# Kernel tuning notes

Hardware: AMD Instinct MI355X
Metric: run time of the kernel (lower is better)

## Reference

```python
import jax, jax.numpy as jnp
import numpy as np
from jax import lax

B, T = 128, 512
V, D = 100000, 100   # word vocab, word embedding dim
H = 100              # per-direction LSTM hidden (concat -> 200)
L = 25               # number of CRF labels


def setup_inputs() -> dict:
    key = jax.random.key(0)
    ks = jax.random.split(key, 16)
    s = 0.02
    inp = {
        "tok_tensor": jax.random.randint(ks[0], (B, T), 0, V, dtype=jnp.int32),
        "tag_tensor": jax.random.randint(ks[1], (B, T), 0, L, dtype=jnp.int32),
        "lengths": jnp.full((B,), T, dtype=jnp.int32),
        "word_emb": jax.random.normal(ks[2], (V, D), jnp.float32) * s,
        # forward-direction LSTM (PyTorch gate order i,f,g,o)
        "w_ih_f": jax.random.normal(ks[3], (4 * H, D), jnp.float32) * s,
        "w_hh_f": jax.random.normal(ks[4], (4 * H, H), jnp.float32) * s,
        "b_ih_f": jax.random.normal(ks[5], (4 * H,), jnp.float32) * s,
        "b_hh_f": jax.random.normal(ks[6], (4 * H,), jnp.float32) * s,
        # backward-direction LSTM
        "w_ih_b": jax.random.normal(ks[7], (4 * H, D), jnp.float32) * s,
        "w_hh_b": jax.random.normal(ks[8], (4 * H, H), jnp.float32) * s,
        "b_ih_b": jax.random.normal(ks[9], (4 * H,), jnp.float32) * s,
        "b_hh_b": jax.random.normal(ks[10], (4 * H,), jnp.float32) * s,
        # hidden2tag linear
        "w_tag": jax.random.normal(ks[11], (L, 2 * H), jnp.float32) * s,
        "b_tag": jax.random.normal(ks[12], (L,), jnp.float32) * s,
        # CRF params
        "transitions": jax.random.normal(ks[13], (L, L), jnp.float32) * 0.1,
        "start_trans": jax.random.normal(ks[14], (L,), jnp.float32) * 0.1,
        "end_trans": jax.random.normal(ks[15], (L,), jnp.float32) * 0.1,
    }
    return inp


def _lstm(x_tbd, w_ih, w_hh, b_ih, b_hh, reverse):
    """x_tbd: [T,B,D] -> hidden states [T,B,H], aligned with input time axis."""
    Bh = x_tbd.shape[1]
    Hh = w_hh.shape[1]
    h0 = jnp.zeros((Bh, Hh), x_tbd.dtype)
    c0 = jnp.zeros((Bh, Hh), x_tbd.dtype)

    def step(carry, xt):
        h, c = carry
        gates = xt @ w_ih.T + b_ih + h @ w_hh.T + b_hh
        i, f, g, o = jnp.split(gates, 4, axis=-1)
        i = jax.nn.sigmoid(i); f = jax.nn.sigmoid(f)
        g = jnp.tanh(g); o = jax.nn.sigmoid(o)
        c = f * c + i * g
        h = o * jnp.tanh(c)
        return (h, c), h

    _, hs = lax.scan(step, (h0, c0), x_tbd, reverse=reverse)
    return hs


def _crf_nll(emissions, tags, mask, transitions, start_trans, end_trans):
    """Sum over batch of -(gold path score - log partition).
    emissions: [B,T,L], tags: [B,T] int, mask: [B,T] float (1=valid)."""
    Bb = emissions.shape[0]
    b_idx = jnp.arange(Bb)
    em_t = emissions.transpose(1, 0, 2)   # [T,B,L]
    tags_t = tags.T                       # [T,B]
    mask_t = mask.T                       # [T,B]

    # --- gold path score ---
    first_tags = tags_t[0]
    score0 = start_trans[first_tags] + em_t[0][b_idx, first_tags]

    def num_step(score, inp):
        em, tp, tc, m = inp  # emissions[t], tags[t-1], tags[t], mask[t]
        s = transitions[tp, tc] + em[b_idx, tc]
        return score + m * s, None

    gold, _ = lax.scan(num_step, score0,
                       (em_t[1:], tags_t[:-1], tags_t[1:], mask_t[1:]))
    last_idx = jnp.sum(mask, axis=1).astype(jnp.int32) - 1
    last_tags = tags[b_idx, last_idx]
    gold = gold + end_trans[last_tags]

    # --- log partition (forward algorithm) ---
    alpha0 = start_trans + em_t[0]  # [B,L]

    def part_step(alpha, inp):
        em, m = inp
        # [B,L_prev,1] + [L_prev,L_next] + [B,1,L_next]
        nxt = jax.nn.logsumexp(alpha[:, :, None] + transitions[None] + em[:, None, :], axis=1)
        alpha = jnp.where(m[:, None] > 0, nxt, alpha)
        return alpha, None

    alpha, _ = lax.scan(part_step, alpha0, (em_t[1:], mask_t[1:]))
    logZ = jax.nn.logsumexp(alpha + end_trans, axis=1)
    return jnp.sum(logZ - gold)


def reference(tok_tensor, tag_tensor, lengths,
              word_emb, w_ih_f, w_hh_f, b_ih_f, b_hh_f,
              w_ih_b, w_hh_b, b_ih_b, b_hh_b,
              w_tag, b_tag, transitions, start_trans, end_trans):
    # word embedding lookup: [B,T,D]
    tok_embs = word_emb[tok_tensor]
    x_tbd = tok_embs.transpose(1, 0, 2)  # [T,B,D]
    # BiLSTM encoder (dropout off: eval / deterministic reference)
    h_fwd = _lstm(x_tbd, w_ih_f, w_hh_f, b_ih_f, b_hh_f, reverse=False)
    h_bwd = _lstm(x_tbd, w_ih_b, w_hh_b, b_ih_b, b_hh_b, reverse=True)
    seq = jnp.concatenate([h_fwd, h_bwd], axis=-1).transpose(1, 0, 2)  # [B,T,2H]
    # hidden2tag
    emissions = jnp.einsum('btd,ld->btl', seq, w_tag) + b_tag  # [B,T,L]
    # CRF negative log-likelihood
    mask = (jnp.arange(T)[None, :] < lengths[:, None]).astype(emissions.dtype)
    return _crf_nll(emissions, tag_tensor, mask, transitions, start_trans, end_trans)
```

## Files before the change

kernel.cpp:

```cpp
#include <hip/hip_runtime.h>
#include <cstdint>
#include <cstddef>

#define BB 128
#define TT 512
#define DD 100
#define HH 100
#define NG 400
#define LL 25
#define TS 32
#define NTILE 16
#define F_LOG2E 1.44269504088896340736f
#define F_LN2   0.69314718055994530942f

typedef __decltype(__builtin_amdgcn_cvt_pkrtz(0.f, 0.f)) h2_t;
typedef _Float16 v8h __attribute__((ext_vector_type(8)));
typedef float v4f __attribute__((ext_vector_type(4)));

__device__ __forceinline__ h2_t bc_h2(unsigned int u) {
  return __builtin_bit_cast(h2_t, u);
}
__device__ __forceinline__ unsigned int pk(float x, float y) {
  return __builtin_bit_cast(unsigned int, __builtin_amdgcn_cvt_pkrtz(x, y));
}

__device__ __forceinline__ float fdot2(h2_t a, h2_t b, float c) {
#if __has_builtin(__builtin_amdgcn_fdot2)
  return __builtin_amdgcn_fdot2(a, b, c, false);
#else
  return c + (float)a[0] * (float)b[0] + (float)a[1] * (float)b[1];
#endif
}

__device__ __forceinline__ float fexp2(float x) { return __builtin_amdgcn_exp2f(x); }
__device__ __forceinline__ float flog2(float x) { return __builtin_amdgcn_logf(x); }
__device__ __forceinline__ float frcp(float x)  { return __builtin_amdgcn_rcpf(x); }

__device__ __forceinline__ float sigmoid_f(float x) {
  return frcp(1.f + fexp2(-F_LOG2E * x));
}
__device__ __forceinline__ float tanh_f(float x) {
  float e = fexp2(2.f * F_LOG2E * x);
  return 1.f - 2.f * frcp(e + 1.f);
}

template <int CTRL>
__device__ __forceinline__ float qadd(float v) {
#if __has_builtin(__builtin_amdgcn_mov_dpp)
  int m = __builtin_amdgcn_mov_dpp(__builtin_bit_cast(int, v), CTRL, 0xF, 0xF, true);
  return v + __builtin_bit_cast(float, m);
#else
  int x = (CTRL == 177) ? 1 : 2;
  return v + __shfl_xor(v, x);
#endif
}

template <int LANE>
__device__ __forceinline__ float qbcast(float v) {
#if __has_builtin(__builtin_amdgcn_mov_dpp)
  int m = __builtin_amdgcn_mov_dpp(__builtin_bit_cast(int, v), LANE * 0x55, 0xF, 0xF, true);
  return __builtin_bit_cast(float, m);
#else
  return __shfl(v, (threadIdx.x & 63 & ~3) + LANE);
#endif
}

__device__ __forceinline__ float rfl(float v) {
  return __builtin_bit_cast(float,
      __builtin_amdgcn_readfirstlane(__builtin_bit_cast(int, v)));
}

__device__ __forceinline__ void wave_fence() {
#if __has_builtin(__builtin_amdgcn_wave_barrier)
  __builtin_amdgcn_wave_barrier();
#endif
}

__device__ __forceinline__ void lds_barrier() {
  __builtin_amdgcn_s_waitcnt(0xC07F);
  __builtin_amdgcn_s_barrier();
}

__global__ __launch_bounds__(512, 2) void lstm_fused3(
    const int* __restrict__ tok, const float* __restrict__ emb,
    const float* __restrict__ w_ih_f, const float* __restrict__ w_ih_b,
    const float* __restrict__ b_ih_f, const float* __restrict__ b_hh_f,
    const float* __restrict__ b_ih_b, const float* __restrict__ b_hh_b,
    const float* __restrict__ w_hh_f, const float* __restrict__ w_hh_b,
    const float* __restrict__ w_tag, const float* __restrict__ b_tag,
    float* __restrict__ em_f, float* __restrict__ em_b)
{
  const int tid = threadIdx.x;
  const int b   = blockIdx.x & 127;
  const int dir = blockIdx.x >> 7;
  const float* w_hh = dir ? w_hh_b : w_hh_f;
  const float* w_ih = dir ? w_ih_b : w_ih_f;
  const float* b_ih = dir ? b_ih_b : b_ih_f;
  const float* b_hh = dir ? b_hh_b : b_hh_f;

  __shared__ __align__(16) unsigned short gin_lds[TS * 400];
  __shared__ __align__(16) unsigned int xlds[TS * 68];
  __shared__ __align__(16) unsigned int hls0[52];
  __shared__ __align__(16) unsigned int hls1[52];

  const int wv   = tid >> 6;
  const int lane = tid & 63;
  const int l16  = lane & 15;
  const int quad = lane >> 4;
  const int c0b  = (25 * wv) >> 3;
  const int c1b  = (25 * (wv + 1)) >> 3;
  const int ncol = c1b - c0b;

  v8h bfr[4][4];
  int pcol[4];
#pragma unroll
  for (int ci = 0; ci < 4; ++ci) {
    const int cc = (ci < ncol) ? (c0b + ci) : c0b;
    const int n  = 16 * cc + l16;
    const float* wr = w_ih + (size_t)n * DD;
#pragma unroll
    for (int f = 0; f < 3; ++f) {
      const float* wp = wr + f * 32 + quad * 8;
      float4 va = *(const float4*)(wp);
      float4 vb = *(const float4*)(wp + 4);
      uint4 u;
      u.x = pk(va.x, va.y); u.y = pk(va.z, va.w);
      u.z = pk(vb.x, vb.y); u.w = pk(vb.z, vb.w);
      bfr[ci][f] = __builtin_bit_cast(v8h, u);
    }
    {
      uint4 u = {0u, 0u, 0u, 0u};
      if (quad == 0) {
        float4 va = *(const float4*)(wr + 96);
        u.x = pk(va.x, va.y); u.y = pk(va.z, va.w);
      }
      bfr[ci][3] = __builtin_bit_cast(v8h, u);
    }
    const int qn = (n * 41) >> 12;
    pcol[ci] = ((n - 100 * qn) << 2) + qn;
  }

  for (int i = tid; i < TS * 18; i += 512) {
    int row = i / 18;
    int d = i - row * 18;
    xlds[row * 68 + 50 + d] = 0u;
  }

  const bool uact = tid < NG;
  const int j = tid >> 2;
  const int s = tid & 3;
  const int od = 12 * s;
  const int nnv = (s == 3) ? 14 : 12;

  h2_t wA[14], wB[14], wC[14], wD[14];
  float bias = 0.f;
  if (uact) {
#pragma unroll
    for (int d = 0; d < 14; ++d) {
      int dd = (d < nnv) ? (od + d) : 0;
      const float* r0 = w_hh + (size_t)(0 * 100 + j) * HH + 2 * dd;
      const float* r1 = w_hh + (size_t)(1 * 100 + j) * HH + 2 * dd;
      const float* r2 = w_hh + (size_t)(2 * 100 + j) * HH + 2 * dd;
      const float* r3 = w_hh + (size_t)(3 * 100 + j) * HH + 2 * dd;
      h2_t z = __builtin_amdgcn_cvt_pkrtz(0.f, 0.f);
      wA[d] = (d < nnv) ? __builtin_amdgcn_cvt_pkrtz(r0[0], r0[1]) : z;
      wB[d] = (d < nnv) ? __builtin_amdgcn_cvt_pkrtz(r1[0], r1[1]) : z;
      wC[d] = (d < nnv) ? __builtin_amdgcn_cvt_pkrtz(r2[0], r2[1]) : z;
      wD[d] = (d < nnv) ? __builtin_amdgcn_cvt_pkrtz(r3[0], r3[1]) : z;
    }
    bias = b_ih[s * 100 + j] + b_hh[s * 100 + j];
  }
  const float kk2 = (s == 2) ? (2.f * F_LOG2E) : (-F_LOG2E);
  const float cA  = (s == 2) ? -2.f : 1.f;
  const float cB  = (s == 2) ? 1.f : 0.f;

  const int el = tid - 448;
  const bool eact = (el >= 0) && (el < 50);
  const int l  = (el >= 0) ? (el >> 1) : 0;
  const int hf = (el >= 0) ? (el & 1) : 0;
  const int eo = hf ? 24 : 0;
  const int en = hf ? 26 : 24;
  h2_t wt[26];
  float bt = 0.f;
  if (eact) {
    const float* wr = w_tag + (size_t)l * 200 + dir * 100;
#pragma unroll
    for (int d = 0; d < 26; ++d) {
      int dd = (d < en) ? (eo + d) : 0;
      h2_t z = __builtin_amdgcn_cvt_pkrtz(0.f, 0.f);
      wt[d] = (d < en) ? __builtin_amdgcn_cvt_pkrtz(wr[2 * dd], wr[2 * dd + 1]) : z;
    }
    if (dir == 0 && hf == 0) bt = b_tag[l];
  }
  float* emo = dir ? em_b : em_f;
  float* emp = emo + ((size_t)b * TT + (dir ? (TT - 1) : 0)) * LL + l;
  const ptrdiff_t estep = dir ? -(ptrdiff_t)LL : (ptrdiff_t)LL;

  if (tid < 52) { hls0[tid] = 0u; hls1[tid] = 0u; }

  const int tprow = tid / 13;
  const int tps   = tid - 13 * tprow;
  const bool tp_act = tid < 416;

  float4 xa = {0, 0, 0, 0}, xb = {0, 0, 0, 0};
  if (tp_act) {
    int ii = tprow;
    int tt = dir ? (TT - 1 - ii) : ii;
    int tk = tok[b * TT + tt];
    const float* xp = emb + (size_t)tk * DD + 8 * tps;
    xa = *(const float4*)xp;
    if (tps < 12) xb = *(const float4*)(xp + 4);
  }

  float c = 0.f;
  unsigned short gnext = 0;
  int grow = 0;

#define SDOT(d, hh) \
  p0 = fdot2(wA[d], bc_h2(hh), p0); p1 = fdot2(wB[d], bc_h2(hh), p1); \
  p2 = fdot2(wC[d], bc_h2(hh), p2); p3 = fdot2(wD[d], bc_h2(hh), p3);
#define EDOT(d, hh) { h2_t h = bc_h2(hh); \
  if ((d & 3) == 0) a0 = fdot2(wt[d], h, a0); \
  else if ((d & 3) == 1) a1 = fdot2(wt[d], h, a1); \
  else if ((d & 3) == 2) a2 = fdot2(wt[d], h, a2); \
  else a3 = fdot2(wt[d], h, a3); }

#define SCAN_STEP(HRD, HWR, TVNZ)                                          \
  {                                                                        \
    if (uact) {                                                            \
      unsigned short gcurr = gnext;                                        \
      int nr = (grow < TS - 1) ? grow + 1 : TS - 1;                        \
      gnext = gin_lds[nr * 400 + tid];                                     \
      grow = nr;                                                           \
      const unsigned int* hp = (HRD) + od;                                 \
      uint4 u0 = *((const uint4*)hp);                                      \
      uint4 u1 = *((const uint4*)(hp + 4));                                \
      uint4 u2 = *((const uint4*)(hp + 8));                                \
      uint2 u3 = *((const uint2*)(hp + 12));                               \
      float p0, p1, p2, p3;                                                \
      p0 = fdot2(wA[0], bc_h2(u0.x), 0.f);                                 \
      p1 = fdot2(wB[0], bc_h2(u0.x), 0.f);                                 \
      p2 = fdot2(wC[0], bc_h2(u0.x), 0.f);                                 \
      p3 = fdot2(wD[0], bc_h2(u0.x), 0.f);                                 \
      SDOT(1, u0.y)  SDOT(2, u0.z)  SDOT(3, u0.w)                          \
      SDOT(4, u1.x)  SDOT(5, u1.y)  SDOT(6, u1.z)  SDOT(7, u1.w)           \
      SDOT(8, u2.x)  SDOT(9, u2.y)  SDOT(10, u2.z) SDOT(11, u2.w)          \
      SDOT(12, u3.x) SDOT(13, u3.y)                                        \
      p0 = qadd<78>(qadd<177>(p0));                                        \
      p1 = qadd<78>(qadd<177>(p1));                                        \
      p2 = qadd<78>(qadd<177>(p2));                                        \
      p3 = qadd<78>(qadd<177>(p3));                                        \
      float psel = (s == 0) ? p0 : (s == 1) ? p1 : (s == 2) ? p2 : p3;     \
      float gate = psel + bias + (float)__builtin_bit_cast(__fp16, gcurr); \
      float y  = fexp2(kk2 * gate);                                        \
      float rr = frcp(1.f + y);                                            \
      float actv = fmaf(cA, rr, cB);                                       \
      float iv = qbcast<0>(actv);                                          \
      float fv = qbcast<1>(actv);                                          \
      float gv = qbcast<2>(actv);                                          \
      float ov = qbcast<3>(actv);                                          \
      c = fmaf(fv, c, iv * gv);                                            \
      float hvv = ov * tanh_f(c);                                          \
      if (s == 0) ((__fp16*)(HWR))[j] = (__fp16)hvv;                       \
    } else if (eact && (TVNZ)) {                                           \
      const unsigned int* hp = (HRD) + eo;                                 \
      uint4 e0 = *((const uint4*)hp);                                      \
      uint4 e1 = *((const uint4*)(hp + 4));                                \
      uint4 e2 = *((const uint4*)(hp + 8));                                \
      uint4 e3 = *((const uint4*)(hp + 12));                               \
      uint4 e4 = *((const uint4*)(hp + 16));                               \
      uint4 e5 = *((const uint4*)(hp + 20));                               \
      uint2 e6 = *((const uint2*)(hp + 24));                               \
      float a0, a1, a2, a3;                                                \
      a0 = fdot2(wt[0], bc_h2(e0.x), 0.f);                                 \
      a1 = fdot2(wt[1], bc_h2(e0.y), 0.f);                                 \
      a2 = fdot2(wt[2], bc_h2(e0.z), 0.f);                                 \
      a3 = fdot2(wt[3], bc_h2(e0.w), 0.f);                                 \
      EDOT(4, e1.x)  EDOT(5, e1.y)  EDOT(6, e1.z)  EDOT(7, e1.w)           \
      EDOT(8, e2.x)  EDOT(9, e2.y)  EDOT(10, e2.z) EDOT(11, e2.w)          \
      EDOT(12, e3.x) EDOT(13, e3.y) EDOT(14, e3.z) EDOT(15, e3.w)          \
      EDOT(16, e4.x) EDOT(17, e4.y) EDOT(18, e4.z) EDOT(19, e4.w)          \
      EDOT(20, e5.x) EDOT(21, e5.y) EDOT(22, e5.z) EDOT(23, e5.w)          \
      EDOT(24, e6.x) EDOT(25, e6.y)                                        \
      float ss = (a0 + a1) + (a2 + a3);                                    \
      float tot = qadd<177>(ss);                                           \
      if (hf == 0) *emp = tot + bt;                                        \
      emp += estep;                                                        \
    }                                                                      \
    lds_barrier();                                                         \
  }

  __syncthreads();

  for (int T = 0; T < NTILE; ++T) {
    if (tp_act) {
      unsigned int* xr = xlds + tprow * 68 + 4 * tps;
      if (tps < 12) {
        uint4 u;
        u.x = pk(xa.x, xa.y); u.y = pk(xa.z, xa.w);
        u.z = pk(xb.x, xb.y); u.w = pk(xb.z, xb.w);
        *(uint4*)xr = u;
      } else {
        xr[0] = pk(xa.x, xa.y);
        xr[1] = pk(xa.z, xa.w);
      }
    }
    __syncthreads();

    {
      v8h af[2][4];
#pragma unroll
      for (int rg = 0; rg < 2; ++rg)
#pragma unroll
        for (int f = 0; f < 4; ++f)
          af[rg][f] = __builtin_bit_cast(v8h,
              *(const uint4*)(xlds + (rg * 16 + l16) * 68 + f * 16 + quad * 4));

      if (tp_act && T + 1 < NTILE) {
        int ii = (T + 1) * TS + tprow;
        int tt = dir ? (TT - 1 - ii) : ii;
        int tk = tok[b * TT + tt];
        const float* xp = emb + (size_t)tk * DD + 8 * tps;
        xa = *(const float4*)xp;
        if (tps < 12) xb = *(const float4*)(xp + 4);
      }

      __fp16* gout = (__fp16*)gin_lds;
#pragma unroll
      for (int ci = 0; ci < 4; ++ci) {
        if (ci >= ncol) break;
        const int p = pcol[ci];
#pragma unroll
        for (int rg = 0; rg < 2; ++rg) {
          v4f acc = {0.f, 0.f, 0.f, 0.f};
          acc = __builtin_amdgcn_mfma_f32_16x16x32_f16(af[rg][0], bfr[ci][0], acc, 0, 0, 0);
          acc = __builtin_amdgcn_mfma_f32_16x16x32_f16(af[rg][1], bfr[ci][1], acc, 0, 0, 0);
          acc = __builtin_amdgcn_mfma_f32_16x16x32_f16(af[rg][2], bfr[ci][2], acc, 0, 0, 0);
          acc = __builtin_amdgcn_mfma_f32_16x16x32_f16(af[rg][3], bfr[ci][3], acc, 0, 0, 0);
          const int rowb = rg * 16 + quad * 4;
#pragma unroll
          for (int r = 0; r < 4; ++r)
            gout[(rowb + r) * 400 + p] = (__fp16)acc[r];
        }
      }
    }
    __syncthreads();
    if (uact) { grow = 0; gnext = gin_lds[tid]; }

    SCAN_STEP(hls0, hls1, (T > 0))
    SCAN_STEP(hls1, hls0, true)
    for (int it = 1; it < TS / 2; ++it) {
      SCAN_STEP(hls0, hls1, true)
      SCAN_STEP(hls1, hls0, true)
    }
  }
#undef SCAN_STEP
#undef SDOT

  if (eact) {
    const unsigned int* hp = hls0 + eo;
    uint4 e0 = *((const uint4*)hp);
    uint4 e1 = *((const uint4*)(hp + 4));
    uint4 e2 = *((const uint4*)(hp + 8));
    uint4 e3 = *((const uint4*)(hp + 12));
    uint4 e4 = *((const uint4*)(hp + 16));
    uint4 e5 = *((const uint4*)(hp + 20));
    uint2 e6 = *((const uint2*)(hp + 24));
    float a0, a1, a2, a3;
    a0 = fdot2(wt[0], bc_h2(e0.x), 0.f);
    a1 = fdot2(wt[1], bc_h2(e0.y), 0.f);
    a2 = fdot2(wt[2], bc_h2(e0.z), 0.f);
    a3 = fdot2(wt[3], bc_h2(e0.w), 0.f);
    EDOT(4, e1.x)  EDOT(5, e1.y)  EDOT(6, e1.z)  EDOT(7, e1.w)
    EDOT(8, e2.x)  EDOT(9, e2.y)  EDOT(10, e2.z) EDOT(11, e2.w)
    EDOT(12, e3.x) EDOT(13, e3.y) EDOT(14, e3.z) EDOT(15, e3.w)
    EDOT(16, e4.x) EDOT(17, e4.y) EDOT(18, e4.z) EDOT(19, e4.w)
    EDOT(20, e5.x) EDOT(21, e5.y) EDOT(22, e5.z) EDOT(23, e5.w)
    EDOT(24, e6.x) EDOT(25, e6.y)
    float ss = (a0 + a1) + (a2 + a3);
    float tot = qadd<177>(ss);
    if (hf == 0) {
      int ttp = dir ? 0 : (TT - 1);
      emo[((size_t)b * TT + ttp) * LL + l] = tot + bt;
    }
  }
#undef EDOT
}

__global__ __launch_bounds__(192) void crf_all2(
    const float* __restrict__ em_f, const float* __restrict__ em_b,
    const int* __restrict__ tags, const int* __restrict__ lengths,
    const float* __restrict__ trans,
    const float* __restrict__ startt, const float* __restrict__ endt,
    float* __restrict__ out)
{
  const int tid = threadIdx.x;
  const int b   = blockIdx.x;
  const int w   = tid >> 6;
  const int lane = tid & 63;

  __shared__ __align__(16) float As[2][32];
  __shared__ float abf[LL], abb[LL];
  __shared__ float gd;

  if (w < 2 && lane >= LL && lane < 32) As[w][lane] = 0.f;

  if (w < 2) {
    const int side = w;
    const int j = (lane < LL) ? lane : 0;
    const float* ef = em_f + (size_t)b * TT * LL;
    const float* eb = em_b + (size_t)b * TT * LL;
    float* Aw = As[side];
    const float4* Ap = (const float4*)Aw;

    float E[28];
#pragma unroll
    for (int i = 0; i < LL; ++i) {
      float tv = (side == 0 ? trans[i * LL + j] : trans[j * LL + i]);
      E[i] = fexp2(tv * F_LOG2E);
    }
    E[25] = 0.f; E[26] = 0.f; E[27] = 0.f;

#define LSE_STEP(vin, aout)                                                \
    {                                                                      \
      float sh = rfl(vin);                                                 \
      C += sh;                                                             \
      float A = fexp2((vin) - sh);                                         \
      if (lane < LL) Aw[lane] = A;                                         \
      wave_fence();                                                        \
      float4 q0 = Ap[0], q1 = Ap[1], q2 = Ap[2], q3 = Ap[3];               \
      float4 q4 = Ap[4], q5 = Ap[5], q6 = Ap[6];                           \
      float s0, s1, s2, s3;                                                \
      s0 = q0.x * E[0];  s1 = q0.y * E[1];                                 \
      s2 = q0.z * E[2];  s3 = q0.w * E[3];                                 \
      s0 = fmaf(q1.x, E[4], s0);  s1 = fmaf(q1.y, E[5], s1);               \
      s2 = fmaf(q1.z, E[6], s2);  s3 = fmaf(q1.w, E[7], s3);               \
      s0 = fmaf(q2.x, E[8], s0);  s1 = fmaf(q2.y, E[9], s1);               \
      s2 = fmaf(q2.z, E[10], s2); s3 = fmaf(q2.w, E[11], s3);              \
      s0 = fmaf(q3.x, E[12], s0); s1 = fmaf(q3.y, E[13], s1);              \
      s2 = fmaf(q3.z, E[14], s2); s3 = fmaf(q3.w, E[15], s3);              \
      s0 = fmaf(q4.x, E[16], s0); s1 = fmaf(q4.y, E[17], s1);              \
      s2 = fmaf(q4.z, E[18], s2); s3 = fmaf(q4.w, E[19], s3);              \
      s0 = fmaf(q5.x, E[20], s0); s1 = fmaf(q5.y, E[21], s1);              \
      s2 = fmaf(q5.z, E[22], s2); s3 = fmaf(q5.w, E[23], s3);              \
      s0 = fmaf(q6.x, E[24], s0); s1 = fmaf(q6.y, E[25], s1);              \
      s2 = fmaf(q6.z, E[26], s2); s3 = fmaf(q6.w, E[27], s3);              \
      aout = flog2((s0 + s1) + (s2 + s3));                                 \
    }

    float a, C = 0.f;
    if (side == 0) {
      a = (startt[j] + ef[j] + eb[j]) * F_LOG2E;
      float efA = ef[LL + j],     ebA = eb[LL + j];
      float efB = ef[2 * LL + j], ebB = eb[2 * LL + j];
      for (int t = 1; t < 256; ++t) {
        float em2 = (efA + ebA) * F_LOG2E;
        int tn = (t + 2 < 256) ? (t + 2) : 255;
        efA = efB; ebA = ebB;
        efB = ef[(size_t)tn * LL + j];
        ebB = eb[(size_t)tn * LL + j];
        float nx;
        LSE_STEP(a, nx)
        a = nx + em2;
      }
    } else {
      a = endt[j] * F_LOG2E;
      float efA = ef[(size_t)(TT - 1) * LL + j], ebA = eb[(size_t)(TT - 1) * LL + j];
      float efB = ef[(size_t)(TT - 2) * LL + j], ebB = eb[(size_t)(TT - 2) * LL + j];
      for (int stpi = 0; stpi < 256; ++stpi) {
        float em2 = (efA + ebA) * F_LOG2E;
        int t1n = (stpi + 2 < 256) ? (TT - 3 - stpi) : 256;
        efA = efB; ebA = ebB;
        efB = ef[(size_t)t1n * LL + j];
        ebB = eb[(size_t)t1n * LL + j];
        float v = a + em2;
        LSE_STEP(v, a)
      }
    }
#undef LSE_STEP
    if (lane < LL) {
      if (side == 0) abf[lane] = a + C;
      else          abb[lane] = a + C;
    }
  } else {
    const int len = lengths[b];
    float acc = 0.f;
#pragma unroll
    for (int k = 0; k < 8; ++k) {
      int t = k * 64 + lane;
      int tg = tags[b * TT + t];
      size_t ei = ((size_t)b * TT + t) * LL + tg;
      float e = em_f[ei] + em_b[ei];
      float term;
      if (t == 0) term = startt[tg] + e;
      else        term = trans[tags[b * TT + t - 1] * LL + tg] + e;
      if (t == len - 1) term += endt[tg];
      if (t < len) acc += term;
    }
    for (int o = 32; o > 0; o >>= 1) acc += __shfl_down(acc, o);
    if (lane == 0) gd = acc;
  }
  __syncthreads();

  if (tid < 64) {
    float v = (tid < LL) ? (abf[tid] + abb[tid]) : -1e30f;
    float m = v;
    for (int o = 32; o > 0; o >>= 1) m = fmaxf(m, __shfl_down(m, o));
    m = rfl(m);
    float e = (tid < LL) ? fexp2(v - m) : 0.f;
    for (int o = 32; o > 0; o >>= 1) e += __shfl_down(e, o);
    if (tid == 0)
      atomicAdd(out, (m + flog2(e)) * F_LN2 - gd);
  }
}

extern "C" void kernel_launch(void* const* d_in, const int* in_sizes, int n_in,
                              void* d_out, int out_size, void* d_ws, size_t ws_size,
                              hipStream_t stream) {
  const int*   tok   = (const int*)d_in[0];
  const int*   tags  = (const int*)d_in[1];
  const int*   lens  = (const int*)d_in[2];
  const float* emb   = (const float*)d_in[3];
  const float* wif   = (const float*)d_in[4];
  const float* whf   = (const float*)d_in[5];
  const float* bif   = (const float*)d_in[6];
  const float* bhf   = (const float*)d_in[7];
  const float* wib   = (const float*)d_in[8];
  const float* whb   = (const float*)d_in[9];
  const float* bib   = (const float*)d_in[10];
  const float* bhb   = (const float*)d_in[11];
  const float* wtag  = (const float*)d_in[12];
  const float* btag  = (const float*)d_in[13];
  const float* trans = (const float*)d_in[14];
  const float* st    = (const float*)d_in[15];
  const float* en    = (const float*)d_in[16];

  char* wsb = (char*)d_ws;
  float* em_f = (float*)wsb;
  float* em_b = (float*)(wsb + 6553600);

  hipMemsetAsync(d_out, 0, sizeof(float), stream);

  lstm_fused3<<<256, 512, 0, stream>>>(tok, emb, wif, wib, bif, bhf, bib, bhb,
                                       whf, whb, wtag, btag, em_f, em_b);
  crf_all2<<<128, 192, 0, stream>>>(em_f, em_b, tags, lens, trans, st, en,
                                    (float*)d_out);
}
```

Measured before the change: 427.2 us.

## Parallelize CRF forward over time chunks via per-chunk transfer matrix products

Replaces the sequential 256-step bidirectional CRF log-partition scan with a chunked approach. Each of 8 time chunks per sentence computes a 25x25 product of scaled exp-transition and emission matrices in its own block. A combine kernel then chains the 8 chunk matrices with per-step exponent renormalization. This trades serial latency for more parallel work and an extra kernel launch. It also works in the linear probability domain with fixed scaling, which risks overflow or underflow and ignores lengths masking in the partition function.

```diff
diff --git a/kernel.cpp b/kernel.cpp
--- a/kernel.cpp
+++ b/kernel.cpp
@@ -387,7 +387,102 @@
 #undef EDOT
 }
 
-__global__ __launch_bounds__(192) void crf_all2(
+#define CHN  8
+#define CLEN 64
+__device__ __align__(16) float g_PT[(size_t)BB * CHN * LL * 28];
+
+__global__ __launch_bounds__(128, 2) void crf_chunks(
+    const float* __restrict__ em_f, const float* __restrict__ em_b,
+    const float* __restrict__ trans)
+{
+  const int tid = threadIdx.x;
+  const int b   = blockIdx.x >> 3;
+  const int c   = blockIdx.x & 7;
+  const int ts  = c * CLEN;
+
+  __shared__ __align__(16) float Al[2][LL][28];
+  __shared__ __align__(16) float el[CLEN][32];
+
+  {
+    const int row  = tid >> 1;
+    const int half = tid & 1;
+    const int jb   = half ? 13 : 0;
+    const int nj   = half ? 12 : 13;
+    const float* pf = em_f + ((size_t)b * TT + ts + row) * LL;
+    const float* pb = em_b + ((size_t)b * TT + ts + row) * LL;
+    for (int q = 0; q < nj; ++q) {
+      int jj = jb + q;
+      el[row][jj] = fexp2((pf[jj] + pb[jj]) * F_LOG2E);
+    }
+  }
+
+  const bool lact = tid < 125;
+  const int i  = tid / 5;
+  const int jg = tid - 5 * i;
+  const int j0 = 5 * jg;
+
+  float E[25][5];
+  if (lact) {
+#pragma unroll
+    for (int k = 0; k < 25; ++k) {
+      const float* tr = trans + k * 25 + j0;
+#pragma unroll
+      for (int u = 0; u < 5; ++u)
+        E[k][u] = fexp2(tr[u] * F_LOG2E - 5.f);
+    }
+#pragma unroll
+    for (int u = 0; u < 5; ++u)
+      Al[0][i][j0 + u] = (i == j0 + u) ? 1.f : 0.f;
+  }
+  __syncthreads();
+
+  int p = 0;
+  const int s0 = (c == 0) ? 1 : 0;
+  for (int st = s0; st < CLEN; ++st) {
+    if (lact) {
+      const float* ar = &Al[p][i][0];
+      float4 q0 = *(const float4*)(ar);
+      float4 q1 = *(const float4*)(ar + 4);
+      float4 q2 = *(const float4*)(ar + 8);
+      float4 q3 = *(const float4*)(ar + 12);
+      float4 q4 = *(const float4*)(ar + 16);
+      float4 q5 = *(const float4*)(ar + 20);
+      float a24 = ar[24];
+      float e0 = el[st][j0];
+      float e1 = el[st][j0 + 1];
+      float e2 = el[st][j0 + 2];
+      float e3 = el[st][j0 + 3];
+      float e4 = el[st][j0 + 4];
+      float av[25] = {q0.x, q0.y, q0.z, q0.w, q1.x, q1.y, q1.z, q1.w,
+                      q2.x, q2.y, q2.z, q2.w, q3.x, q3.y, q3.z, q3.w,
+                      q4.x, q4.y, q4.z, q4.w, q5.x, q5.y, q5.z, q5.w, a24};
+      float c0 = 0.f, c1 = 0.f, c2 = 0.f, c3 = 0.f, c4 = 0.f;
+#pragma unroll
+      for (int k = 0; k < 25; ++k) {
+        float avk = av[k];
+        c0 = fmaf(avk, E[k][0], c0);
+        c1 = fmaf(avk, E[k][1], c1);
+        c2 = fmaf(avk, E[k][2], c2);
+        c3 = fmaf(avk, E[k][3], c3);
+        c4 = fmaf(avk, E[k][4], c4);
+      }
+      float* wr = &Al[p ^ 1][i][j0];
+      wr[0] = c0 * e0; wr[1] = c1 * e1; wr[2] = c2 * e2;
+      wr[3] = c3 * e3; wr[4] = c4 * e4;
+    }
+    __syncthreads();
+    p ^= 1;
+  }
+
+  if (lact) {
+    const size_t base = ((size_t)(b * CHN + c)) * LL;
+#pragma unroll
+    for (int u = 0; u < 5; ++u)
+      g_PT[(base + (j0 + u)) * 28 + i] = Al[p][i][j0 + u];
+  }
+}
+
+__global__ __launch_bounds__(128) void crf_combine(
     const float* __restrict__ em_f, const float* __restrict__ em_b,
     const int* __restrict__ tags, const int* __restrict__ lengths,
     const float* __restrict__ trans,
@@ -396,93 +491,61 @@
 {
   const int tid = threadIdx.x;
   const int b   = blockIdx.x;
-  const int w   = tid >> 6;
-  const int lane = tid & 63;
-
-  __shared__ __align__(16) float As[2][32];
-  __shared__ float abf[LL], abb[LL];
-  __shared__ float gd;
-
-  if (w < 2 && lane >= LL && lane < 32) As[w][lane] = 0.f;
-
-  if (w < 2) {
-    const int side = w;
+
+  __shared__ __align__(16) float Vs[28];
+
+  if (tid < 64) {
+    const int lane = tid;
     const int j = (lane < LL) ? lane : 0;
-    const float* ef = em_f + (size_t)b * TT * LL;
-    const float* eb = em_b + (size_t)b * TT * LL;
-    float* Aw = As[side];
-    const float4* Ap = (const float4*)Aw;
-
-    float E[28];
-#pragma unroll
-    for (int i = 0; i < LL; ++i) {
-      float tv = (side == 0 ? trans[i * LL + j] : trans[j * LL + i]);
-      E[i] = fexp2(tv * F_LOG2E);
-    }
-    E[25] = 0.f; E[26] = 0.f; E[27] = 0.f;
-
-#define LSE_STEP(vin, aout)                                                \
-    {                                                                      \
-      float sh = rfl(vin);                                                 \
-      C += sh;                                                             \
-      float A = fexp2((vin) - sh);                                         \
-      if (lane < LL) Aw[lane] = A;                                         \
-      wave_fence();                                                        \
-      float4 q0 = Ap[0], q1 = Ap[1], q2 = Ap[2], q3 = Ap[3];               \
-      float4 q4 = Ap[4], q5 = Ap[5], q6 = Ap[6];                           \
-      float s0, s1, s2, s3;                                                \
-      s0 = q0.x * E[0];  s1 = q0.y * E[1];                                 \
-      s2 = q0.z * E[2];  s3 = q0.w * E[3];                                 \
-      s0 = fmaf(q1.x, E[4], s0);  s1 = fmaf(q1.y, E[5], s1);               \
-      s2 = fmaf(q1.z, E[6], s2);  s3 = fmaf(q1.w, E[7], s3);               \
-      s0 = fmaf(q2.x, E[8], s0);  s1 = fmaf(q2.y, E[9], s1);               \
-      s2 = fmaf(q2.z, E[10], s2); s3 = fmaf(q2.w, E[11], s3);              \
-      s0 = fmaf(q3.x, E[12], s0); s1 = fmaf(q3.y, E[13], s1);              \
-      s2 = fmaf(q3.z, E[14], s2); s3 = fmaf(q3.w, E[15], s3);              \
-      s0 = fmaf(q4.x, E[16], s0); s1 = fmaf(q4.y, E[17], s1);              \
-      s2 = fmaf(q4.z, E[18], s2); s3 = fmaf(q4.w, E[19], s3);              \
-      s0 = fmaf(q5.x, E[20], s0); s1 = fmaf(q5.y, E[21], s1);              \
-      s2 = fmaf(q5.z, E[22], s2); s3 = fmaf(q5.w, E[23], s3);              \
-      s0 = fmaf(q6.x, E[24], s0); s1 = fmaf(q6.y, E[25], s1);              \
-      s2 = fmaf(q6.z, E[26], s2); s3 = fmaf(q6.w, E[27], s3);              \
-      aout = flog2((s0 + s1) + (s2 + s3));                                 \
-    }
-
-    float a, C = 0.f;
-    if (side == 0) {
-      a = (startt[j] + ef[j] + eb[j]) * F_LOG2E;
-      float efA = ef[LL + j],     ebA = eb[LL + j];
-      float efB = ef[2 * LL + j], ebB = eb[2 * LL + j];
-      for (int t = 1; t < 256; ++t) {
-        float em2 = (efA + ebA) * F_LOG2E;
-        int tn = (t + 2 < 256) ? (t + 2) : 255;
-        efA = efB; ebA = ebB;
-        efB = ef[(size_t)tn * LL + j];
-        ebB = eb[(size_t)tn * LL + j];
-        float nx;
-        LSE_STEP(a, nx)
-        a = nx + em2;
-      }
-    } else {
-      a = endt[j] * F_LOG2E;
-      float efA = ef[(size_t)(TT - 1) * LL + j], ebA = eb[(size_t)(TT - 1) * LL + j];
-      float efB = ef[(size_t)(TT - 2) * LL + j], ebB = eb[(size_t)(TT - 2) * LL + j];
-      for (int stpi = 0; stpi < 256; ++stpi) {
-        float em2 = (efA + ebA) * F_LOG2E;
-        int t1n = (stpi + 2 < 256) ? (TT - 3 - stpi) : 256;
-        efA = efB; ebA = ebB;
-        efB = ef[(size_t)t1n * LL + j];
-        ebB = eb[(size_t)t1n * LL + j];
-        float v = a + em2;
-        LSE_STEP(v, a)
-      }
-    }
-#undef LSE_STEP
-    if (lane < LL) {
-      if (side == 0) abf[lane] = a + C;
-      else          abb[lane] = a + C;
-    }
+    const float* ef0 = em_f + (size_t)b * TT * LL;
+    const float* eb0 = em_b + (size_t)b * TT * LL;
+    float v = fexp2((startt[j] + ef0[j] + eb0[j]) * F_LOG2E);
+    float C = 0.f;
+    for (int c = 0; c < CHN; ++c) {
+      if (lane < LL) Vs[lane] = v;
+      wave_fence();
+      float4 s0 = *(const float4*)(Vs);
+      float4 s1 = *(const float4*)(Vs + 4);
+      float4 s2 = *(const float4*)(Vs + 8);
+      float4 s3 = *(const float4*)(Vs + 12);
+      float4 s4 = *(const float4*)(Vs + 16);
+      float4 s5 = *(const float4*)(Vs + 20);
+      float s24 = Vs[24];
+      wave_fence();
+      const float* pr = g_PT + ((size_t)(b * CHN + c) * LL + j) * 28;
+      float4 p0 = *(const float4*)(pr);
+      float4 p1 = *(const float4*)(pr + 4);
+      float4 p2 = *(const float4*)(pr + 8);
+      float4 p3 = *(const float4*)(pr + 12);
+      float4 p4 = *(const float4*)(pr + 16);
+      float4 p5 = *(const float4*)(pr + 20);
+      float p24 = pr[24];
+      float nv = s0.x * p0.x;
+      nv = fmaf(s0.y, p0.y, nv); nv = fmaf(s0.z, p0.z, nv); nv = fmaf(s0.w, p0.w, nv);
+      nv = fmaf(s1.x, p1.x, nv); nv = fmaf(s1.y, p1.y, nv);
+      nv = fmaf(s1.z, p1.z, nv); nv = fmaf(s1.w, p1.w, nv);
+      nv = fmaf(s2.x, p2.x, nv); nv = fmaf(s2.y, p2.y, nv);
+      nv = fmaf(s2.z, p2.z, nv); nv = fmaf(s2.w, p2.w, nv);
+      nv = fmaf(s3.x, p3.x, nv); nv = fmaf(s3.y, p3.y, nv);
+      nv = fmaf(s3.z, p3.z, nv); nv = fmaf(s3.w, p3.w, nv);
+      nv = fmaf(s4.x, p4.x, nv); nv = fmaf(s4.y, p4.y, nv);
+      nv = fmaf(s4.z, p4.z, nv); nv = fmaf(s4.w, p4.w, nv);
+      nv = fmaf(s5.x, p5.x, nv); nv = fmaf(s5.y, p5.y, nv);
+      nv = fmaf(s5.z, p5.z, nv); nv = fmaf(s5.w, p5.w, nv);
+      nv = fmaf(s24, p24, nv);
+      float nv0 = rfl(nv);
+      int k = ((__builtin_bit_cast(int, nv0) >> 23) & 255) - 127;
+      k = (k > 100) ? 100 : ((k < -100) ? -100 : k);
+      float scl = __builtin_bit_cast(float, (127 - k) << 23);
+      v = nv * scl;
+      C += (float)k;
+    }
+    float term = (lane < LL) ? v * fexp2(endt[j] * F_LOG2E) : 0.f;
+    for (int o = 32; o > 0; o >>= 1) term += __shfl_down(term, o);
+    if (lane == 0)
+      atomicAdd(out, (flog2(term) + C + 5.f * 511.f) * F_LN2);
   } else {
+    const int lane = tid & 63;
     const int len = lengths[b];
     float acc = 0.f;
 #pragma unroll
@@ -498,19 +561,7 @@
       if (t < len) acc += term;
     }
     for (int o = 32; o > 0; o >>= 1) acc += __shfl_down(acc, o);
-    if (lane == 0) gd = acc;
-  }
-  __syncthreads();
-
-  if (tid < 64) {
-    float v = (tid < LL) ? (abf[tid] + abb[tid]) : -1e30f;
-    float m = v;
-    for (int o = 32; o > 0; o >>= 1) m = fmaxf(m, __shfl_down(m, o));
-    m = rfl(m);
-    float e = (tid < LL) ? fexp2(v - m) : 0.f;
-    for (int o = 32; o > 0; o >>= 1) e += __shfl_down(e, o);
-    if (tid == 0)
-      atomicAdd(out, (m + flog2(e)) * F_LN2 - gd);
+    if (lane == 0) atomicAdd(out, -acc);
   }
 }
 
@@ -543,6 +594,7 @@
 
   lstm_fused3<<<256, 512, 0, stream>>>(tok, emb, wif, wib, bif, bhf, bib, bhb,
                                        whf, whb, wtag, btag, em_f, em_b);
-  crf_all2<<<128, 192, 0, stream>>>(em_f, em_b, tags, lens, trans, st, en,
-                                    (float*)d_out);
-}
+  crf_chunks<<<BB * CHN, 128, 0, stream>>>(em_f, em_b, trans);
+  crf_combine<<<BB, 128, 0, stream>>>(em_f, em_b, tags, lens, trans, st, en,
+                                      (float*)d_out);
+}
```

Measured after the change: 426.9 us. No clear change (-0.1%).
